# Performance work log

Measured on AMD Instinct MI355X. Metric: run time of the kernel, lower is better.

Reference implementation:

```python
import jax, jax.numpy as jnp
import numpy as np
from jax import lax

B, E, DIN = 16, 1024, 128   # batch, num_edges, link_state_dim
P, D = 2048, 128            # num_paths, path_state_dim


def _topology():
    # deterministic ragged paths: lengths in [4,16], at least one of max length 16
    lengths = 4 + (np.arange(P) % 13)
    idx = np.repeat(np.arange(P), lengths).astype(np.int32)          # path id per entry
    seqs = np.concatenate([np.arange(l) for l in lengths]).astype(np.int32)  # position in path
    paths = np.random.RandomState(0).randint(0, E, size=idx.shape[0]).astype(np.int32)
    return paths, idx, seqs


def setup_inputs() -> dict:
    key = jax.random.key(0)
    ks = jax.random.split(key, 8)
    paths, idx, seqs = _topology()
    s_in = 1.0 / np.sqrt(DIN)
    s_h = 1.0 / np.sqrt(D)
    return dict(
        inputs=jax.random.normal(ks[0], (B, E, DIN), jnp.float32),
        W_in=jax.random.normal(ks[1], (DIN, 3 * D), jnp.float32) * s_in,
        W_rec=jax.random.normal(ks[2], (D, 3 * D), jnp.float32) * s_h,
        b_in=jnp.zeros((3 * D,), jnp.float32),
        b_rec=jnp.zeros((3 * D,), jnp.float32),
        wq=jax.random.normal(ks[3], (D, D), jnp.float32) * s_h,
        wk=jax.random.normal(ks[4], (D, D), jnp.float32) * s_h,
        wv=jax.random.normal(ks[5], (D, D), jnp.float32) * s_h,
        paths=paths, idx=idx, seqs=seqs,
    )


def _forward(inputs, W_in, W_rec, b_in, b_rec, wq, wk, wv, paths, idx, seqs, max_len):
    Bc = inputs.shape[0]
    # --- ragged gather -> dense zero-padded tensor [B, P, max_len, DIN] (tf.gather + scatter_nd) ---
    h_tild = inputs[:, paths]                                  # [B, n_entries, DIN]
    link = jnp.zeros((Bc, P, max_len, DIN), inputs.dtype)
    link = link.at[:, idx, seqs].set(h_tild)
    x = link.reshape(Bc * P, max_len, DIN)                     # [BP, L, DIN]
    # --- GRU over time (keras GRUCell default: reset_after=True, tanh/sigmoid) ---
    xg = jnp.einsum('nld,de->lne', x, W_in) + b_in             # [L, BP, 3D]
    h0 = jnp.zeros((Bc * P, D), inputs.dtype)

    def step(h, xg_t):
        hg = h @ W_rec + b_rec                                 # [BP, 3D]
        xz, xr, xh = jnp.split(xg_t, 3, axis=-1)
        hz, hr, hh = jnp.split(hg, 3, axis=-1)
        z = jax.nn.sigmoid(xz + hz)
        r = jax.nn.sigmoid(xr + hr)
        hc = jnp.tanh(xh + r * hh)
        hn = z * h + (1.0 - z) * hc
        return hn, hn

    last, hs = lax.scan(step, h0, xg)                          # last:[BP,D], hs:[L,BP,D]
    hs = jnp.transpose(hs, (1, 0, 2))                          # [BP, L, D]
    # --- single-query QKV attention (raw scores, no softmax, as in source) ---
    key_ = hs @ wk                                             # [BP, L, D]
    val = hs @ wv                                              # [BP, L, D]
    q = last @ wq                                              # [BP, D]
    att = jnp.einsum('nld,nd->nl', key_, q)                    # [BP, L]
    ctx = jnp.einsum('nl,nld->nd', att, val)                   # [BP, D]
    return ctx.reshape(Bc, P, D)


def reference(inputs, W_in, W_rec, b_in, b_rec, wq, wk, wv, paths, idx, seqs):
    max_len = int(np.max(np.asarray(seqs))) + 1                # static (16)
    return _forward(inputs, W_in, W_rec, b_in, b_rec, wq, wk, wv, paths, idx, seqs, max_len)
```

## Files before the change

### kernel.cpp

```cpp
#include <hip/hip_runtime.h>
#include <hip/hip_bf16.h>
#include <cstddef>

#define P_ 2048
#define B_ 16
#define E_ 1024
#define D_ 128
#define L_ 16
#define TD_ 384

typedef _Float16 f16x2 __attribute__((ext_vector_type(2)));
typedef _Float16 f16x8 __attribute__((ext_vector_type(8)));
typedef float    f32x4 __attribute__((ext_vector_type(4)));

__device__ __forceinline__ unsigned short f2h(float x) {
    _Float16 h = (_Float16)x;
    return __builtin_bit_cast(unsigned short, h);
}
__device__ __forceinline__ unsigned pk2(float a, float b) {
    return __builtin_bit_cast(unsigned, __builtin_amdgcn_cvt_pkrtz(a, b));
}
__device__ __forceinline__ float lo16(unsigned u) {
    return (float)__builtin_bit_cast(f16x2, u)[0];
}
__device__ __forceinline__ float hi16(unsigned u) {
    return (float)__builtin_bit_cast(f16x2, u)[1];
}
__device__ __forceinline__ float dot2w(unsigned hu, unsigned qu, float c) {
#if __has_builtin(__builtin_amdgcn_fdot2)
    typedef __fp16 h2v __attribute__((ext_vector_type(2)));
    return __builtin_amdgcn_fdot2(__builtin_bit_cast(h2v, hu),
                                  __builtin_bit_cast(h2v, qu), c, false);
#else
    f16x2 h = __builtin_bit_cast(f16x2, hu), q = __builtin_bit_cast(f16x2, qu);
    return c + (float)h[0] * (float)q[0] + (float)h[1] * (float)q[1];
#endif
}

__device__ __forceinline__ void wf16(const float* __restrict__ src,
                                     unsigned short* __restrict__ dst, int g, int N) {
    int lane = g & 63, kt = (g >> 6) & 3, tile = g >> 8;
    int k0 = kt * 32 + (lane >> 4) * 8;
    int c = tile * 16 + (lane & 15);
#pragma unroll
    for (int j = 0; j < 8; ++j)
        dst[(size_t)g * 8 + j] = f2h(src[(size_t)(k0 + j) * N + c]);
}

__global__ __launch_bounds__(256) void k_prep(const float* __restrict__ W_rec,
                                              const float* __restrict__ W_in,
                                              const float* __restrict__ wq,
                                              const float* __restrict__ wk,
                                              const float* __restrict__ wv,
                                              int* __restrict__ pt,
                                              unsigned short* __restrict__ WfR,
                                              unsigned short* __restrict__ WfI,
                                              unsigned short* __restrict__ wvf,
                                              float* __restrict__ M) {
    __shared__ float wk_lds[128 * 129];
    __shared__ float wq_row2[2][128];
    int blk = blockIdx.x, tid = threadIdx.x;
    if      (blk < 128) { pt[blk * 256 + tid] = E_; return; }
    else if (blk < 152) { wf16(W_rec, WfR, (blk - 128) * 256 + tid, TD_); return; }
    else if (blk < 176) { wf16(W_in,  WfI, (blk - 152) * 256 + tid, TD_); return; }
    else if (blk < 184) { wf16(wv,    wvf, (blk - 176) * 256 + tid, 128); return; }
    int j0 = (blk - 184) * 2;
    int d = tid & 127, half = tid >> 7;
    for (int r = half * 64; r < half * 64 + 64; ++r)
        wk_lds[r * 129 + d] = wk[r * 128 + d];
    wq_row2[half][d] = wq[(j0 + half) * 128 + d];
    __syncthreads();
    float acc = 0.f;
    for (int k = 0; k < 128; ++k) acc += wq_row2[half][k] * wk_lds[d * 129 + k];
    M[(j0 + half) * 128 + d] = acc;
}

__global__ __launch_bounds__(256) void k_G(const float* __restrict__ inputs,
                                           const unsigned short* __restrict__ WfI,
                                           const float* __restrict__ b_in,
                                           const float* __restrict__ b_rec,
                                           unsigned short* __restrict__ G2,
                                           const int* __restrict__ paths,
                                           const int* __restrict__ idx,
                                           const int* __restrict__ seqs, int J, int scatB,
                                           int* __restrict__ pt,
                                           const float* __restrict__ M,
                                           unsigned short* __restrict__ Mf) {
    if (blockIdx.x >= 1024) {
        int tb = blockIdx.x - 1024;
        if (tb < scatB) {
            int j = tb * 256 + threadIdx.x;
            if (j < J) pt[idx[j] * L_ + seqs[j]] = paths[j];
        } else if (tb < scatB + 8) {
            wf16(M, Mf, (tb - scatB) * 256 + threadIdx.x, 128);
        } else {
            for (int i = threadIdx.x; i < 2048; i += 256) {
                int bx = i >> 7, cc = i & 127;
                size_t base = ((size_t)(bx * (E_ + 1) + E_) * 128 + cc) * 4;
                G2[base]     = f2h(b_in[cc] + b_rec[cc]);
                G2[base + 1] = f2h(b_in[128 + cc] + b_rec[128 + cc]);
                G2[base + 2] = f2h(b_in[256 + cc]);
                G2[base + 3] = 0;
            }
        }
        return;
    }
    __shared__ __align__(16) unsigned short a_lds[16][136];
    int tid = threadIdx.x, w = tid >> 6, L = tid & 63;
    int l15 = L & 15, q = L >> 4;
    int row0 = blockIdx.x * 16;
    int badd = row0 >> 10;
    {
        int r = tid >> 4, c = (tid & 15) * 8;
        const float4* p = (const float4*)(inputs + (size_t)(row0 + r) * 128 + c);
        float4 v0 = p[0], v1 = p[1];
        uint4 st;
        st.x = pk2(v0.x, v0.y); st.y = pk2(v0.z, v0.w);
        st.z = pk2(v1.x, v1.y); st.w = pk2(v1.z, v1.w);
        *(uint4*)&a_lds[r][c] = st;
    }
    __syncthreads();
    f16x8 af[4];
#pragma unroll
    for (int kt = 0; kt < 4; ++kt)
        af[kt] = *(const f16x8*)&a_lds[l15][kt * 32 + q * 8];
#pragma unroll
    for (int ct = 0; ct < 6; ++ct) {
        int tl = 6 * w + ct;
        f32x4 acc = (f32x4){0.f, 0.f, 0.f, 0.f};
#pragma unroll
        for (int kt = 0; kt < 4; ++kt)
            acc = __builtin_amdgcn_mfma_f32_16x16x32_f16(
                af[kt], *(const f16x8*)(WfI + (size_t)((tl * 4 + kt) * 64 + L) * 8), acc, 0, 0, 0);
        int g  = tl >> 3;
        int dd = (tl & 7) * 16 + l15;
        float bia = b_in[tl * 16 + l15] + (g < 2 ? b_rec[tl * 16 + l15] : 0.f);
#pragma unroll
        for (int j = 0; j < 4; ++j) {
            int r = q * 4 + j;
            G2[((size_t)(row0 + r + badd) * 128 + dd) * 4 + g] = f2h(acc[j] + bia);
        }
    }
}

__global__ __launch_bounds__(512, 4) void k_rec(const unsigned short* __restrict__ WfR,
                                                const float* __restrict__ b_rec,
                                                const unsigned short* __restrict__ G2,
                                                const int* __restrict__ pt,
                                                const unsigned short* __restrict__ Mf,
                                                const unsigned short* __restrict__ wvf,
                                                float* __restrict__ out) {
    __shared__ __align__(16) unsigned short hsl[16][16][136];
    __shared__ __align__(16) unsigned short qkb[16][136];
    __shared__ __align__(16) unsigned short svb[16][136];
    __shared__ float attp[2][16][16];
    __shared__ int ofs_lds[16][16];

    int tid = threadIdx.x, w = tid >> 6, L = tid & 63;
    int l15 = L & 15, q = L >> 4;
    int c0 = 16 * w + 4 * q;
    int n0 = blockIdx.x * 16;
    int b  = n0 >> 11;
    int p0 = n0 & (P_ - 1);
    int bb = b * (E_ + 1);

    f16x8 afw[3][4];
#pragma unroll
    for (int g = 0; g < 3; ++g)
#pragma unroll
        for (int kt = 0; kt < 4; ++kt)
            afw[g][kt] = *(const f16x8*)(WfR + (size_t)(((g * 8 + w) * 4 + kt) * 64 + L) * 8);

    if (tid < 256)
        ofs_lds[tid >> 4][tid & 15] = (bb + pt[p0 * L_ + tid]) << 10;

    f32x4 rh4;
#pragma unroll
    for (int j = 0; j < 4; ++j) rh4[j] = b_rec[256 + c0 + j];
    float h_reg[4] = {0.f, 0.f, 0.f, 0.f};
    __syncthreads();

    int ofs[16];
    {
        const uint4* op = (const uint4*)&ofs_lds[l15][0];
        uint4 o0 = op[0], o1 = op[1], o2 = op[2], o3 = op[3];
        ofs[0]  = o0.x; ofs[1]  = o0.y; ofs[2]  = o0.z; ofs[3]  = o0.w;
        ofs[4]  = o1.x; ofs[5]  = o1.y; ofs[6]  = o1.z; ofs[7]  = o1.w;
        ofs[8]  = o2.x; ofs[9]  = o2.y; ofs[10] = o2.z; ofs[11] = o2.w;
        ofs[12] = o3.x; ofs[13] = o3.y; ofs[14] = o3.z; ofs[15] = o3.w;
    }

    const char* g2c = (const char*)G2 + (size_t)c0 * 8;
    uint4 cur0 = *(const uint4*)(g2c + ofs[0]);
    uint4 cur1 = *(const uint4*)(g2c + ofs[0] + 16);

#pragma unroll
    for (int t = 0; t < L_; ++t) {
        uint4 nx0 = cur0, nx1 = cur1;
        if (t < 15) {
            const char* gp = g2c + ofs[t + 1];
            nx0 = *(const uint4*)(gp);
            nx1 = *(const uint4*)(gp + 16);
        }

        float xh[4];
        f32x4 acc[3];
        acc[0][0] = lo16(cur0.x); acc[0][1] = lo16(cur0.z);
        acc[0][2] = lo16(cur1.x); acc[0][3] = lo16(cur1.z);
        acc[1][0] = hi16(cur0.x); acc[1][1] = hi16(cur0.z);
        acc[1][2] = hi16(cur1.x); acc[1][3] = hi16(cur1.z);
        xh[0] = lo16(cur0.y); xh[1] = lo16(cur0.w);
        xh[2] = lo16(cur1.y); xh[3] = lo16(cur1.w);
        acc[2] = rh4;

        if (t > 0) {
            f16x8 hf[4];
#pragma unroll
            for (int kt = 0; kt < 4; ++kt)
                hf[kt] = *(const f16x8*)&hsl[t - 1][l15][kt * 32 + q * 8];
#pragma unroll
            for (int g = 0; g < 3; ++g)
#pragma unroll
                for (int kt = 0; kt < 4; ++kt)
                    acc[g] = __builtin_amdgcn_mfma_f32_16x16x32_f16(afw[g][kt], hf[kt], acc[g], 0, 0, 0);
        }

        float hn[4];
#pragma unroll
        for (int j = 0; j < 4; ++j) {
            float z   = __builtin_amdgcn_rcpf(1.f + __expf(-acc[0][j]));
            float rg  = __builtin_amdgcn_rcpf(1.f + __expf(-acc[1][j]));
            float pre = xh[j] + rg * acc[2][j];
            float hc  = 1.f - 2.f * __builtin_amdgcn_rcpf(__expf(2.f * pre) + 1.f);
            hn[j] = hc + z * (h_reg[j] - hc);
            h_reg[j] = hn[j];
        }
        uint2 st;
        st.x = pk2(hn[0], hn[1]); st.y = pk2(hn[2], hn[3]);
        *(uint2*)&hsl[t][l15][c0] = st;
        cur0 = nx0; cur1 = nx1;

        __builtin_amdgcn_wave_barrier();
        __builtin_amdgcn_s_waitcnt(0xC07F);
        __builtin_amdgcn_s_barrier();
        __builtin_amdgcn_wave_barrier();
    }

    {
        f16x8 hf[4];
#pragma unroll
        for (int kt = 0; kt < 4; ++kt)
            hf[kt] = *(const f16x8*)&hsl[15][l15][kt * 32 + q * 8];
        f32x4 a = (f32x4){0.f, 0.f, 0.f, 0.f};
#pragma unroll
        for (int kt = 0; kt < 4; ++kt)
            a = __builtin_amdgcn_mfma_f32_16x16x32_f16(
                *(const f16x8*)(Mf + (size_t)((w * 4 + kt) * 64 + L) * 8), hf[kt], a, 0, 0, 0);
        uint2 st;
        st.x = pk2(a[0], a[1]); st.y = pk2(a[2], a[3]);
        *(uint2*)&qkb[l15][c0] = st;
    }
    __syncthreads();

    {
        int s = tid & 15, l = (tid >> 4) & 15, half = tid >> 8;
        const uint4* hr = (const uint4*)&hsl[l][s][half * 64];
        const uint4* qr = (const uint4*)&qkb[s][half * 64];
        float a = 0.f;
#pragma unroll
        for (int k8 = 0; k8 < 8; ++k8) {
            uint4 hh = hr[k8], qq = qr[k8];
            a = dot2w(hh.x, qq.x, a); a = dot2w(hh.y, qq.y, a);
            a = dot2w(hh.z, qq.z, a); a = dot2w(hh.w, qq.w, a);
        }
        attp[half][s][l] = a;
    }
    __syncthreads();

    {
        int s = tid >> 5, d0 = (tid & 31) * 4;
        float v[4] = {0.f, 0.f, 0.f, 0.f};
#pragma unroll
        for (int l = 0; l < 16; ++l) {
            float a = attp[0][s][l] + attp[1][s][l];
            uint2 hu = *(const uint2*)&hsl[l][s][d0];
            v[0] += a * lo16(hu.x); v[1] += a * hi16(hu.x);
            v[2] += a * lo16(hu.y); v[3] += a * hi16(hu.y);
        }
        uint2 st;
        st.x = pk2(v[0], v[1]); st.y = pk2(v[2], v[3]);
        *(uint2*)&svb[s][d0] = st;
    }
    __syncthreads();

    {
        f16x8 sf[4];
#pragma unroll
        for (int kt = 0; kt < 4; ++kt)
            sf[kt] = *(const f16x8*)&svb[l15][kt * 32 + q * 8];
        f32x4 a = (f32x4){0.f, 0.f, 0.f, 0.f};
#pragma unroll
        for (int kt = 0; kt < 4; ++kt)
            a = __builtin_amdgcn_mfma_f32_16x16x32_f16(
                *(const f16x8*)(wvf + (size_t)((w * 4 + kt) * 64 + L) * 8), sf[kt], a, 0, 0, 0);
        *(f32x4*)&out[(size_t)(n0 + l15) * D_ + c0] = a;
    }
}

extern "C" void kernel_launch(void* const* d_in, const int* in_sizes, int n_in,
                              void* d_out, int out_size, void* d_ws, size_t ws_size,
                              hipStream_t stream) {
    const float* inputs = (const float*)d_in[0];
    const float* W_in   = (const float*)d_in[1];
    const float* W_rec  = (const float*)d_in[2];
    const float* b_in   = (const float*)d_in[3];
    const float* b_rec  = (const float*)d_in[4];
    const float* wq     = (const float*)d_in[5];
    const float* wk     = (const float*)d_in[6];
    const float* wvp    = (const float*)d_in[7];
    const int* paths    = (const int*)d_in[8];
    const int* idx      = (const int*)d_in[9];
    const int* seqs     = (const int*)d_in[10];
    int J = in_sizes[8];

    const size_t off_pt  = 0;
    const size_t off_WfR = off_pt  + (size_t)P_ * L_ * 4;
    const size_t off_WfI = off_WfR + (size_t)24 * 256 * 16;
    const size_t off_Mf  = off_WfI + (size_t)24 * 256 * 16;
    const size_t off_wvf = off_Mf  + (size_t)8 * 256 * 16;
    const size_t off_M   = off_wvf + (size_t)8 * 256 * 16;
    const size_t off_G2  = off_M   + (size_t)128 * 128 * 4;
    char* ws = (char*)d_ws;
    int* pt             = (int*)(ws + off_pt);
    unsigned short* WfR = (unsigned short*)(ws + off_WfR);
    unsigned short* WfI = (unsigned short*)(ws + off_WfI);
    unsigned short* Mf  = (unsigned short*)(ws + off_Mf);
    unsigned short* wvf = (unsigned short*)(ws + off_wvf);
    float* M            = (float*)(ws + off_M);
    unsigned short* G2  = (unsigned short*)(ws + off_G2);
    float* out = (float*)d_out;

    int scatB = (J + 255) / 256;
    k_prep<<<dim3(248), dim3(256), 0, stream>>>(W_rec, W_in, wq, wk, wvp, pt,
                                                WfR, WfI, wvf, M);
    k_G<<<dim3(1024 + scatB + 8 + 1), dim3(256), 0, stream>>>(inputs, WfI, b_in, b_rec,
                                                              G2, paths, idx, seqs, J,
                                                              scatB, pt, M, Mf);
    k_rec<<<dim3(B_ * P_ / 16), dim3(512), 0, stream>>>(WfR, b_rec, G2, pt,
                                                        Mf, wvf, out);
}
```

Before: 179.1 us.

## Drop precomputed wq·wkᵀ matrix; apply wq and wk separately in recurrence kernel

Removes the fp32 wq·wkᵀ product computed in k_prep, which used a large LDS tile and serial dot products, along with its fp16 conversion pass in k_G. k_rec now applies wq and a transposed wk as two chained MFMA stages through an extra LDS buffer and barrier. k_G is also restructured to compute the z/r/h gate tiles together and write packed 16-byte G2 stores, with biases staged in LDS, replacing scattered 2-byte stores. The trade is shorter prep kernels and coalesced writes in exchange for extra per-block matmul work and a synchronization in k_rec.

```diff
diff --git a/kernel.cpp b/kernel.cpp
--- a/kernel.cpp
+++ b/kernel.cpp
@@ -46,6 +46,15 @@
     for (int j = 0; j < 8; ++j)
         dst[(size_t)g * 8 + j] = f2h(src[(size_t)(k0 + j) * N + c]);
 }
+__device__ __forceinline__ void wfT16(const float* __restrict__ src,
+                                      unsigned short* __restrict__ dst, int g) {
+    int lane = g & 63, kt = (g >> 6) & 3, tile = g >> 8;
+    int k0 = kt * 32 + (lane >> 4) * 8;
+    int m = tile * 16 + (lane & 15);
+#pragma unroll
+    for (int j = 0; j < 8; ++j)
+        dst[(size_t)g * 8 + j] = f2h(src[(size_t)m * 128 + k0 + j]);
+}
 
 __global__ __launch_bounds__(256) void k_prep(const float* __restrict__ W_rec,
                                               const float* __restrict__ W_in,
@@ -55,24 +64,16 @@
                                               int* __restrict__ pt,
                                               unsigned short* __restrict__ WfR,
                                               unsigned short* __restrict__ WfI,
-                                              unsigned short* __restrict__ wvf,
-                                              float* __restrict__ M) {
-    __shared__ float wk_lds[128 * 129];
-    __shared__ float wq_row2[2][128];
+                                              unsigned short* __restrict__ wqf,
+                                              unsigned short* __restrict__ wkTf,
+                                              unsigned short* __restrict__ wvf) {
     int blk = blockIdx.x, tid = threadIdx.x;
-    if      (blk < 128) { pt[blk * 256 + tid] = E_; return; }
-    else if (blk < 152) { wf16(W_rec, WfR, (blk - 128) * 256 + tid, TD_); return; }
-    else if (blk < 176) { wf16(W_in,  WfI, (blk - 152) * 256 + tid, TD_); return; }
-    else if (blk < 184) { wf16(wv,    wvf, (blk - 176) * 256 + tid, 128); return; }
-    int j0 = (blk - 184) * 2;
-    int d = tid & 127, half = tid >> 7;
-    for (int r = half * 64; r < half * 64 + 64; ++r)
-        wk_lds[r * 129 + d] = wk[r * 128 + d];
-    wq_row2[half][d] = wq[(j0 + half) * 128 + d];
-    __syncthreads();
-    float acc = 0.f;
-    for (int k = 0; k < 128; ++k) acc += wq_row2[half][k] * wk_lds[d * 129 + k];
-    M[(j0 + half) * 128 + d] = acc;
+    if      (blk < 128) pt[blk * 256 + tid] = E_;
+    else if (blk < 152) wf16(W_rec, WfR, (blk - 128) * 256 + tid, TD_);
+    else if (blk < 176) wf16(W_in,  WfI, (blk - 152) * 256 + tid, TD_);
+    else if (blk < 184) wf16(wq,    wqf, (blk - 176) * 256 + tid, 128);
+    else if (blk < 192) wfT16(wk,  wkTf, (blk - 184) * 256 + tid);
+    else                wf16(wv,    wvf, (blk - 192) * 256 + tid, 128);
 }
 
 __global__ __launch_bounds__(256) void k_G(const float* __restrict__ inputs,
@@ -83,16 +84,12 @@
                                            const int* __restrict__ paths,
                                            const int* __restrict__ idx,
                                            const int* __restrict__ seqs, int J, int scatB,
-                                           int* __restrict__ pt,
-                                           const float* __restrict__ M,
-                                           unsigned short* __restrict__ Mf) {
+                                           int* __restrict__ pt) {
     if (blockIdx.x >= 1024) {
         int tb = blockIdx.x - 1024;
         if (tb < scatB) {
             int j = tb * 256 + threadIdx.x;
             if (j < J) pt[idx[j] * L_ + seqs[j]] = paths[j];
-        } else if (tb < scatB + 8) {
-            wf16(M, Mf, (tb - scatB) * 256 + threadIdx.x, 128);
         } else {
             for (int i = threadIdx.x; i < 2048; i += 256) {
                 int bx = i >> 7, cc = i & 127;
@@ -106,40 +103,59 @@
         return;
     }
     __shared__ __align__(16) unsigned short a_lds[16][136];
+    __shared__ float bz_l[128], br_l[128], bh_l[128];
     int tid = threadIdx.x, w = tid >> 6, L = tid & 63;
     int l15 = L & 15, q = L >> 4;
     int row0 = blockIdx.x * 16;
     int badd = row0 >> 10;
     {
-        int r = tid >> 4, c = (tid & 15) * 8;
-        const float4* p = (const float4*)(inputs + (size_t)(row0 + r) * 128 + c);
+        int r = tid >> 4, cc = (tid & 15) * 8;
+        const float4* p = (const float4*)(inputs + (size_t)(row0 + r) * 128 + cc);
         float4 v0 = p[0], v1 = p[1];
         uint4 st;
         st.x = pk2(v0.x, v0.y); st.y = pk2(v0.z, v0.w);
         st.z = pk2(v1.x, v1.y); st.w = pk2(v1.z, v1.w);
-        *(uint4*)&a_lds[r][c] = st;
-    }
-    __syncthreads();
-    f16x8 af[4];
+        *(uint4*)&a_lds[r][cc] = st;
+    }
+    if (tid < 128) {
+        bz_l[tid] = b_in[tid] + b_rec[tid];
+        br_l[tid] = b_in[128 + tid] + b_rec[128 + tid];
+        bh_l[tid] = b_in[256 + tid];
+    }
+    __syncthreads();
+
+    f16x8 bf[4];
 #pragma unroll
     for (int kt = 0; kt < 4; ++kt)
-        af[kt] = *(const f16x8*)&a_lds[l15][kt * 32 + q * 8];
-#pragma unroll
-    for (int ct = 0; ct < 6; ++ct) {
-        int tl = 6 * w + ct;
-        f32x4 acc = (f32x4){0.f, 0.f, 0.f, 0.f};
-#pragma unroll
-        for (int kt = 0; kt < 4; ++kt)
-            acc = __builtin_amdgcn_mfma_f32_16x16x32_f16(
-                af[kt], *(const f16x8*)(WfI + (size_t)((tl * 4 + kt) * 64 + L) * 8), acc, 0, 0, 0);
-        int g  = tl >> 3;
-        int dd = (tl & 7) * 16 + l15;
-        float bia = b_in[tl * 16 + l15] + (g < 2 ? b_rec[tl * 16 + l15] : 0.f);
-#pragma unroll
-        for (int j = 0; j < 4; ++j) {
-            int r = q * 4 + j;
-            G2[((size_t)(row0 + r + badd) * 128 + dd) * 4 + g] = f2h(acc[j] + bia);
-        }
+        bf[kt] = *(const f16x8*)&a_lds[l15][kt * 32 + q * 8];
+
+    size_t rowbase = (size_t)(row0 + l15 + badd) * 1024;
+#pragma unroll
+    for (int ct = 0; ct < 2; ++ct) {
+        int tz = 2 * w + ct, tr = 8 + 2 * w + ct, th = 16 + 2 * w + ct;
+        f32x4 az = (f32x4){0.f,0.f,0.f,0.f}, ar = az, ah = az;
+#pragma unroll
+        for (int kt = 0; kt < 4; ++kt) {
+            az = __builtin_amdgcn_mfma_f32_16x16x32_f16(
+                *(const f16x8*)(WfI + (size_t)((tz * 4 + kt) * 64 + L) * 8), bf[kt], az, 0, 0, 0);
+            ar = __builtin_amdgcn_mfma_f32_16x16x32_f16(
+                *(const f16x8*)(WfI + (size_t)((tr * 4 + kt) * 64 + L) * 8), bf[kt], ar, 0, 0, 0);
+            ah = __builtin_amdgcn_mfma_f32_16x16x32_f16(
+                *(const f16x8*)(WfI + (size_t)((th * 4 + kt) * 64 + L) * 8), bf[kt], ah, 0, 0, 0);
+        }
+        int col0 = 32 * w + 16 * ct + 4 * q;
+        uint4 s0, s1;
+        s0.x = pk2(az[0] + bz_l[col0],     ar[0] + br_l[col0]);
+        s0.y = pk2(ah[0] + bh_l[col0],     0.f);
+        s0.z = pk2(az[1] + bz_l[col0 + 1], ar[1] + br_l[col0 + 1]);
+        s0.w = pk2(ah[1] + bh_l[col0 + 1], 0.f);
+        s1.x = pk2(az[2] + bz_l[col0 + 2], ar[2] + br_l[col0 + 2]);
+        s1.y = pk2(ah[2] + bh_l[col0 + 2], 0.f);
+        s1.z = pk2(az[3] + bz_l[col0 + 3], ar[3] + br_l[col0 + 3]);
+        s1.w = pk2(ah[3] + bh_l[col0 + 3], 0.f);
+        char* gp = (char*)G2 + rowbase + (size_t)col0 * 8;
+        *(uint4*)gp = s0;
+        *(uint4*)(gp + 16) = s1;
     }
 }
 
@@ -147,7 +163,8 @@
                                                 const float* __restrict__ b_rec,
                                                 const unsigned short* __restrict__ G2,
                                                 const int* __restrict__ pt,
-                                                const unsigned short* __restrict__ Mf,
+                                                const unsigned short* __restrict__ wqf,
+                                                const unsigned short* __restrict__ wkTf,
                                                 const unsigned short* __restrict__ wvf,
                                                 float* __restrict__ out) {
     __shared__ __align__(16) unsigned short hsl[16][16][136];
@@ -255,7 +272,23 @@
 #pragma unroll
         for (int kt = 0; kt < 4; ++kt)
             a = __builtin_amdgcn_mfma_f32_16x16x32_f16(
-                *(const f16x8*)(Mf + (size_t)((w * 4 + kt) * 64 + L) * 8), hf[kt], a, 0, 0, 0);
+                *(const f16x8*)(wqf + (size_t)((w * 4 + kt) * 64 + L) * 8), hf[kt], a, 0, 0, 0);
+        uint2 st;
+        st.x = pk2(a[0], a[1]); st.y = pk2(a[2], a[3]);
+        *(uint2*)&svb[l15][c0] = st;
+    }
+    __syncthreads();
+
+    {
+        f16x8 uf[4];
+#pragma unroll
+        for (int kt = 0; kt < 4; ++kt)
+            uf[kt] = *(const f16x8*)&svb[l15][kt * 32 + q * 8];
+        f32x4 a = (f32x4){0.f, 0.f, 0.f, 0.f};
+#pragma unroll
+        for (int kt = 0; kt < 4; ++kt)
+            a = __builtin_amdgcn_mfma_f32_16x16x32_f16(
+                *(const f16x8*)(wkTf + (size_t)((w * 4 + kt) * 64 + L) * 8), uf[kt], a, 0, 0, 0);
         uint2 st;
         st.x = pk2(a[0], a[1]); st.y = pk2(a[2], a[3]);
         *(uint2*)&qkb[l15][c0] = st;
@@ -323,29 +356,29 @@
     const int* seqs     = (const int*)d_in[10];
     int J = in_sizes[8];
 
-    const size_t off_pt  = 0;
-    const size_t off_WfR = off_pt  + (size_t)P_ * L_ * 4;
-    const size_t off_WfI = off_WfR + (size_t)24 * 256 * 16;
-    const size_t off_Mf  = off_WfI + (size_t)24 * 256 * 16;
-    const size_t off_wvf = off_Mf  + (size_t)8 * 256 * 16;
-    const size_t off_M   = off_wvf + (size_t)8 * 256 * 16;
-    const size_t off_G2  = off_M   + (size_t)128 * 128 * 4;
+    const size_t off_pt   = 0;
+    const size_t off_WfR  = off_pt   + (size_t)P_ * L_ * 4;
+    const size_t off_WfI  = off_WfR  + (size_t)24 * 256 * 16;
+    const size_t off_wqf  = off_WfI  + (size_t)24 * 256 * 16;
+    const size_t off_wkTf = off_wqf  + (size_t)8 * 256 * 16;
+    const size_t off_wvf  = off_wkTf + (size_t)8 * 256 * 16;
+    const size_t off_G2   = off_wvf  + (size_t)8 * 256 * 16;
     char* ws = (char*)d_ws;
-    int* pt             = (int*)(ws + off_pt);
-    unsigned short* WfR = (unsigned short*)(ws + off_WfR);
-    unsigned short* WfI = (unsigned short*)(ws + off_WfI);
-    unsigned short* Mf  = (unsigned short*)(ws + off_Mf);
-    unsigned short* wvf = (unsigned short*)(ws + off_wvf);
-    float* M            = (float*)(ws + off_M);
-    unsigned short* G2  = (unsigned short*)(ws + off_G2);
+    int* pt              = (int*)(ws + off_pt);
+    unsigned short* WfR  = (unsigned short*)(ws + off_WfR);
+    unsigned short* WfI  = (unsigned short*)(ws + off_WfI);
+    unsigned short* wqf  = (unsigned short*)(ws + off_wqf);
+    unsigned short* wkTf = (unsigned short*)(ws + off_wkTf);
+    unsigned short* wvf  = (unsigned short*)(ws + off_wvf);
+    unsigned short* G2   = (unsigned short*)(ws + off_G2);
     float* out = (float*)d_out;
 
     int scatB = (J + 255) / 256;
-    k_prep<<<dim3(248), dim3(256), 0, stream>>>(W_rec, W_in, wq, wk, wvp, pt,
-                                                WfR, WfI, wvf, M);
-    k_G<<<dim3(1024 + scatB + 8 + 1), dim3(256), 0, stream>>>(inputs, WfI, b_in, b_rec,
-                                                              G2, paths, idx, seqs, J,
-                                                              scatB, pt, M, Mf);
+    k_prep<<<dim3(200), dim3(256), 0, stream>>>(W_rec, W_in, wq, wk, wvp, pt,
+                                                WfR, WfI, wqf, wkTf, wvf);
+    k_G<<<dim3(1024 + scatB + 1), dim3(256), 0, stream>>>(inputs, WfI, b_in, b_rec,
+                                                          G2, paths, idx, seqs, J,
+                                                          scatB, pt);
     k_rec<<<dim3(B_ * P_ / 16), dim3(512), 0, stream>>>(WfR, b_rec, G2, pt,
-                                                        Mf, wvf, out);
-}
+                                                        wqf, wkTf, wvf, out);
+}
```

After: 181.2 us. About the same (+1.2%).
